# Optimization experiments

Hardware: AMD Instinct MI355X
Metric: run time of the kernel (lower is better)

Reference implementation:

```python
import jax, jax.numpy as jnp
import numpy as np

NUM_HEADS = 16

def setup_inputs() -> dict:
    key = jax.random.key(0)
    ks = jax.random.split(key, 5)
    B, T, C = 2, 2048, 1024
    s = 0.02
    return {
        "x": jax.random.normal(ks[0], (B, T, C), dtype=jnp.float32),
        "attn_w": jax.random.normal(ks[1], (3 * C, C), dtype=jnp.float32) * s,
        "attn_b": jax.random.normal(ks[2], (3 * C,), dtype=jnp.float32) * s,
        "proj_w": jax.random.normal(ks[3], (C, C), dtype=jnp.float32) * s,
        "proj_b": jax.random.normal(ks[4], (C,), dtype=jnp.float32) * s,
    }

def reference(x, attn_w, attn_b, proj_w, proj_b):
    B, T, C = x.shape
    H = NUM_HEADS
    D = C // H
    # fused QKV projection (torch Linear: x @ W^T + b)
    qkv = x @ attn_w.T + attn_b                      # [B, T, 3C]
    q, k, v = jnp.split(qkv, 3, axis=-1)             # each [B, T, C]
    # split heads -> [B, H, T, D]
    def heads(t):
        return t.reshape(B, T, H, D).transpose(0, 2, 1, 3)
    q, k, v = heads(q), heads(k), heads(v)
    scale = 1.0 / jnp.sqrt(jnp.asarray(D, dtype=x.dtype))
    scores = jnp.einsum("bhtd,bhsd->bhts", q, k) * scale   # [B, H, T, T]
    causal = jnp.tril(jnp.ones((T, T), dtype=bool))
    scores = jnp.where(causal[None, None], scores, jnp.asarray(-jnp.inf, dtype=scores.dtype))
    att = jax.nn.softmax(scores, axis=-1)
    out = jnp.einsum("bhts,bhsd->bhtd", att, v)      # [B, H, T, D]
    out = out.transpose(0, 2, 1, 3).reshape(B, T, C)
    return out @ proj_w.T + proj_b
```

## Files before the change

### kernel.cpp

```cpp
#include <hip/hip_runtime.h>
#include <hip/hip_bf16.h>

typedef __bf16 bf16_t;
typedef __bf16 bf16x4 __attribute__((ext_vector_type(4)));
typedef __bf16 bf16x8 __attribute__((ext_vector_type(8)));
typedef float f32x4 __attribute__((ext_vector_type(4)));
typedef float f32x8 __attribute__((ext_vector_type(8)));

#define MFMA16(a, b, c) __builtin_amdgcn_mfma_f32_16x16x32_bf16(a, b, c, 0, 0, 0)

#define GLOAD_LDS16(g, l)                                              \
  __builtin_amdgcn_global_load_lds(                                    \
      (const __attribute__((address_space(1))) unsigned int*)(g),      \
      (__attribute__((address_space(3))) unsigned int*)(l), 16, 0, 0)

constexpr int B = 2, T = 2048, C = 1024, H = 16, D = 64;
constexpr int NQKV = 3 * C;
constexpr int M = B * T;

#define QSCALE 0.18033688011112042f

struct LoOn  { static constexpr bool value = true;  };
struct LoOff { static constexpr bool value = false; };

__global__ __launch_bounds__(256) void cvt_kernel(
    const float* __restrict__ s0, bf16_t* __restrict__ d0, int n0,
    const float* __restrict__ s1, bf16_t* __restrict__ d1, int n1,
    const float* __restrict__ s2, bf16_t* __restrict__ d2, int n2)
{
  const float* s; bf16_t* d; int n;
  if (blockIdx.y == 0)      { s = s0; d = d0; n = n0; }
  else if (blockIdx.y == 1) { s = s1; d = d1; n = n1; }
  else                      { s = s2; d = d2; n = n2; }
  const int idx = (blockIdx.x * 256 + threadIdx.x) * 8;
  if (idx >= n) return;
  f32x8 t = *(const f32x8*)(s + idx);
  bf16x8 r;
#pragma unroll
  for (int j = 0; j < 8; ++j) r[j] = (bf16_t)t[j];
  *(bf16x8*)(d + idx) = r;
}

template<int BM, int BN, int MI, int NI, int WM, int WN>
__device__ __forceinline__ void gemm_mainloop_db(
    const bf16_t* __restrict__ A, const bf16_t* __restrict__ Wt,
    const int K, const int m0, const int n0,
    bf16_t* ldsA0, bf16_t* ldsA1, bf16_t* ldsB0, bf16_t* ldsB1,
    f32x4 acc[MI][NI])
{
  const int tid  = threadIdx.x;
  const int wv   = tid >> 6;
  const int lane = tid & 63;
  const int col  = lane & 15;
  const int quad = lane >> 4;
  const int lr8  = lane >> 3;
  const int cpos = lane & 7;
  const int wm = wv / WN, wn = wv % WN;
  constexpr int NW  = WM * WN;
  constexpr int ARW = BM / NW;
  constexpr int AJ  = ARW / 8;
  constexpr int BRW = BN / NW;
  constexpr int BJ  = BRW / 8;

  const bf16_t* ag[AJ]; const bf16_t* bg[BJ];
#pragma unroll
  for (int j = 0; j < AJ; ++j)
    ag[j] = A + (size_t)(m0 + wv * ARW + j * 8 + lr8) * K + (cpos ^ lr8) * 8;
#pragma unroll
  for (int j = 0; j < BJ; ++j)
    bg[j] = Wt + (size_t)(n0 + wv * BRW + j * 8 + lr8) * K + (cpos ^ lr8) * 8;

  const int xa = quad ^ (col & 7);
  const int niter = K / 64;

#pragma unroll
  for (int j = 0; j < AJ; ++j)
    GLOAD_LDS16(ag[j], ldsA0 + (wv * ARW + j * 8) * 64);
#pragma unroll
  for (int j = 0; j < BJ; ++j)
    GLOAD_LDS16(bg[j], ldsB0 + (wv * BRW + j * 8) * 64);

  for (int it = 0; it < niter; ++it) {
    __syncthreads();
    const bf16_t* cA = (it & 1) ? ldsA1 : ldsA0;
    const bf16_t* cB = (it & 1) ? ldsB1 : ldsB0;
    if (it + 1 < niter) {
      bf16_t* nA = (it & 1) ? ldsA0 : ldsA1;
      bf16_t* nB = (it & 1) ? ldsB0 : ldsB1;
      const int off = (it + 1) * 64;
#pragma unroll
      for (int j = 0; j < AJ; ++j)
        GLOAD_LDS16(ag[j] + off, nA + (wv * ARW + j * 8) * 64);
#pragma unroll
      for (int j = 0; j < BJ; ++j)
        GLOAD_LDS16(bg[j] + off, nB + (wv * BRW + j * 8) * 64);
    }
#pragma unroll
    for (int ks = 0; ks < 2; ++ks) {
      const int xk = (xa ^ (ks * 4)) * 8;
      bf16x8 af[MI], bfr[NI];
#pragma unroll
      for (int mi = 0; mi < MI; ++mi)
        af[mi] = *(const bf16x8*)(cA + (wm * (MI * 16) + mi * 16 + col) * 64 + xk);
#pragma unroll
      for (int ni = 0; ni < NI; ++ni)
        bfr[ni] = *(const bf16x8*)(cB + (wn * (NI * 16) + ni * 16 + col) * 64 + xk);
#pragma unroll
      for (int mi = 0; mi < MI; ++mi)
#pragma unroll
        for (int ni = 0; ni < NI; ++ni)
          acc[mi][ni] = MFMA16(af[mi], bfr[ni], acc[mi][ni]);
    }
  }
}

__global__ __launch_bounds__(256) void qkv_gemm_kernel(
    const bf16_t* __restrict__ x, const bf16_t* __restrict__ w,
    const float* __restrict__ bias,
    bf16_t* __restrict__ qws, bf16_t* __restrict__ kws, bf16_t* __restrict__ vws)
{
  __shared__ __align__(16) bf16_t ldsA[2][128 * 64];
  __shared__ __align__(16) bf16_t ldsB[2][128 * 64];
  const unsigned id = blockIdx.x;
  const unsigned lo = id & 7;
  const unsigned hi = id >> 3;
  const unsigned bx = hi % 24;
  const unsigned by = lo + 8 * (hi / 24);
  const int lane = threadIdx.x & 63;
  const int wv   = threadIdx.x >> 6;
  const int col  = lane & 15;
  const int quad = lane >> 4;
  const int wm = wv >> 1, wn = wv & 1;
  const int m0 = by * 128;
  const int n0 = bx * 128;

  f32x4 acc[4][4] = {};
  gemm_mainloop_db<128, 128, 4, 4, 2, 2>(x, w, C, m0, n0,
                                         ldsA[0], ldsA[1], ldsB[0], ldsB[1], acc);

  const int which = n0 >> 10;

  if (which == 2) {
    __syncthreads();
    bf16_t* vt = &ldsA[0][0] + wv * 4096;

#pragma unroll
    for (int ni = 0; ni < 4; ++ni) {
      const int n = n0 + wn * 64 + ni * 16 + col;
      const float bval = bias[n];
      const int dl = ni * 16 + col;
#pragma unroll
      for (int r = 0; r < 4; ++r) {
        bf16x4 pw;
#pragma unroll
        for (int mi = 0; mi < 4; ++mi)
          pw[mi] = (bf16_t)(acc[mi][ni][r] + bval);
        const int k = 2 * quad + (r >> 1);
        const int S = dl * 8 + (k ^ (dl & 7));
        *(bf16x4*)(vt + S * 8 + (r & 1) * 4) = pw;
      }
    }

    const int b   = (m0 + wm * 64) >> 11;
    const int t0w = (m0 + wm * 64) & (T - 1);
    const int h   = ((n0 + wn * 64) & (C - 1)) >> 6;
    const size_t bh = (size_t)(b * H + h);
    const int lr8 = lane >> 3;
    const int c8  = lane & 7;
#pragma unroll
    for (int j = 0; j < 8; ++j) {
      const int dl = j * 8 + lr8;
      const int d  = dl;
      bf16x8 row = *(const bf16x8*)(vt + (dl * 8 + (c8 ^ (dl & 7))) * 8);
      *(bf16x8*)(vws + (bh * D + d) * T + t0w + c8 * 8) = row;
    }
  } else {
#pragma unroll
    for (int ni = 0; ni < 4; ++ni) {
      const int n = n0 + wn * 64 + ni * 16 + col;
      const float bval = bias[n];
      const int c = n & (C - 1);
      const int h = c >> 6;
      const int d = c & 63;
#pragma unroll
      for (int mi = 0; mi < 4; ++mi) {
#pragma unroll
        for (int r = 0; r < 4; ++r) {
          const int m = m0 + wm * 64 + mi * 16 + quad * 4 + r;
          const int b = m >> 11;
          const int t = m & (T - 1);
          const size_t bh = (size_t)(b * H + h);
          if (which == 0)
            qws[(bh * T + t) * D + d] = (bf16_t)((acc[mi][ni][r] + bval) * QSCALE);
          else
            kws[(bh * T + t) * D + d] = (bf16_t)(acc[mi][ni][r] + bval);
        }
      }
    }
  }
}

__global__ __launch_bounds__(256) void attn_kernel(
    const bf16_t* __restrict__ qws, const bf16_t* __restrict__ kws,
    const bf16_t* __restrict__ vws, bf16_t* __restrict__ yws)
{
  const unsigned id = blockIdx.x;
  const int bh = (id & 7) + 8 * (id >> 7);
  const int pr = (id >> 3) & 15;
  const int tid  = threadIdx.x;
  const int wv   = tid >> 6;
  const int lane = tid & 63;
  const int col  = lane & 15;
  const int quad = lane >> 4;

  const bf16_t* Q  = qws + (size_t)bh * T * D;
  const bf16_t* K  = kws + (size_t)bh * T * D;
  const bf16_t* Vt = vws + (size_t)bh * D * T;

  __shared__ __align__(16) bf16_t ldsK[2][64 * 64];
  __shared__ __align__(16) bf16_t ldsV[2][64 * 64];
  __shared__ __align__(16) bf16_t ldsPh_s[4][16 * 64];
  __shared__ __align__(16) bf16_t ldsPl_s[4][16 * 64];
  bf16_t* ldsPh = ldsPh_s[wv];
  bf16_t* ldsPl = ldsPl_s[wv];

  const int xs   = col & 7;
  const int cxq  = (quad ^ xs) * 8;
  const int lr8  = lane >> 3;
  const int ksrc = (lane & 7) ^ lr8;
  const int pxor = (quad & 1) * 4;
  const int b = bh >> 4;
  const int h = bh & 15;

  const int qt_h = 31 - pr, qt_l = pr;
  const int t0h = qt_h * 64, t0l = qt_l * 64;
  const int twh = t0h + 16 * wv, twl = t0l + 16 * wv;

  bf16x8 qfh0 = *(const bf16x8*)(Q + (size_t)(twh + col) * D + quad * 8);
  bf16x8 qfh1 = *(const bf16x8*)(Q + (size_t)(twh + col) * D + 32 + quad * 8);
  bf16x8 qfl0 = *(const bf16x8*)(Q + (size_t)(twl + col) * D + quad * 8);
  bf16x8 qfl1 = *(const bf16x8*)(Q + (size_t)(twl + col) * D + 32 + quad * 8);

  f32x4 oh[4] = {}, ol[4] = {};
  f32x4 lph = {}, lpl = {};

  auto stage = [&](int it) {
    const int sn = it * 64;
    bf16_t* dK = ldsK[it & 1];
    bf16_t* dV = ldsV[it & 1];
#pragma unroll
    for (int j = 0; j < 2; ++j) {
      GLOAD_LDS16(K + (size_t)(sn + 16 * wv + j * 8 + lr8) * D + ksrc * 8,
                  dK + (16 * wv + j * 8) * 64);
      GLOAD_LDS16(Vt + (size_t)(16 * wv + j * 8 + lr8) * T + sn + ksrc * 8,
                  dV + (16 * wv + j * 8) * 64);
    }
  };

  auto body = [&](auto LOC, const bf16_t* bK, const bf16_t* bV,
                  int s0, bool hdiag, bool ldiag) {
    constexpr bool LO = decltype(LOC)::value;
    f32x4 sch[4], scl[4];
    __builtin_amdgcn_s_setprio(1);
#pragma unroll
    for (int kb = 0; kb < 4; ++kb) {
      const bf16_t* kr = bK + (kb * 16 + col) * 64;
      bf16x8 kf0 = *(const bf16x8*)(kr + cxq);
      bf16x8 kf1 = *(const bf16x8*)(kr + (cxq ^ 32));
      f32x4 a = {};
      a = MFMA16(qfh0, kf0, a);
      a = MFMA16(qfh1, kf1, a);
      sch[kb] = a;
      if constexpr (LO) {
        f32x4 c = {};
        c = MFMA16(qfl0, kf0, c);
        c = MFMA16(qfl1, kf1, c);
        scl[kb] = c;
      }
    }
    __builtin_amdgcn_s_setprio(0);
#pragma unroll
    for (int r = 0; r < 4; ++r) {
      const int prow = (quad * 4 + r) * 64;
      const int pxr  = pxor + r;
      const int poff = prow + (((col >> 1) ^ pxr) * 8) + (col & 1) * 4;
      bf16x4 pw;
#pragma unroll
      for (int kb = 0; kb < 4; ++kb) {
        float p = __builtin_amdgcn_exp2f(sch[kb][r]);
        if (hdiag && (s0 + kb * 16 + col > twh + quad * 4 + r)) p = 0.0f;
        lph[r] += p;
        pw[kb] = (bf16_t)p;
      }
      *(bf16x4*)(ldsPh + poff) = pw;
      if constexpr (LO) {
        bf16x4 pl;
#pragma unroll
        for (int kb = 0; kb < 4; ++kb) {
          float p = __builtin_amdgcn_exp2f(scl[kb][r]);
          if (ldiag && (s0 + kb * 16 + col > twl + quad * 4 + r)) p = 0.0f;
          lpl[r] += p;
          pl[kb] = (bf16_t)p;
        }
        *(bf16x4*)(ldsPl + poff) = pl;
      }
    }
    __builtin_amdgcn_s_setprio(1);
#pragma unroll
    for (int ks = 0; ks < 2; ++ks) {
      const int xk = cxq ^ (ks * 32);
      bf16x8 pah = *(const bf16x8*)(ldsPh + col * 64 + xk);
      bf16x8 pal{};
      if constexpr (LO) pal = *(const bf16x8*)(ldsPl + col * 64 + xk);
#pragma unroll
      for (int ni = 0; ni < 4; ++ni) {
        bf16x8 vf = *(const bf16x8*)(bV + (ni * 16 + col) * 64 + xk);
        oh[ni] = MFMA16(pah, vf, oh[ni]);
        if constexpr (LO) ol[ni] = MFMA16(pal, vf, ol[ni]);
      }
    }
    __builtin_amdgcn_s_setprio(0);
  };

  stage(0);

  for (int it = 0; it < qt_l; ++it) {
    __syncthreads();
    stage(it + 1);
    body(LoOn{}, ldsK[it & 1], ldsV[it & 1], it * 64, false, false);
  }
  {
    const int it = qt_l;
    __syncthreads();
    stage(it + 1);
    body(LoOn{}, ldsK[it & 1], ldsV[it & 1], it * 64, false, true);
  }
  for (int it = qt_l + 1; it < qt_h; ++it) {
    __syncthreads();
    stage(it + 1);
    body(LoOff{}, ldsK[it & 1], ldsV[it & 1], it * 64, false, false);
  }
  {
    __syncthreads();
    body(LoOff{}, ldsK[qt_h & 1], ldsV[qt_h & 1], qt_h * 64, true, false);
  }

#pragma unroll
  for (int r = 0; r < 4; ++r) {
    float l0 = lph[r], l1 = lpl[r];
#pragma unroll
    for (int off = 1; off < 16; off <<= 1) {
      l0 += __shfl_xor(l0, off);
      l1 += __shfl_xor(l1, off);
    }
    const float rl0 = 1.0f / l0, rl1 = 1.0f / l1;
    const int th = twh + quad * 4 + r;
    const int tl = twl + quad * 4 + r;
#pragma unroll
    for (int ni = 0; ni < 4; ++ni) {
      const int d = ni * 16 + col;
      yws[((size_t)(b * T + th)) * C + h * D + d] = (bf16_t)(oh[ni][r] * rl0);
      yws[((size_t)(b * T + tl)) * C + h * D + d] = (bf16_t)(ol[ni][r] * rl1);
    }
  }
}

__global__ __launch_bounds__(256) void proj_gemm_kernel(
    const bf16_t* __restrict__ y, const bf16_t* __restrict__ w,
    const float* __restrict__ bias, float* __restrict__ out)
{
  __shared__ __align__(16) bf16_t ldsA[2][128 * 64];
  __shared__ __align__(16) bf16_t ldsB[2][64 * 64];
  const unsigned id = blockIdx.x;
  const unsigned lo = id & 7;
  const unsigned hi = id >> 3;
  const unsigned bx = hi & 15;
  const unsigned by = lo + 8 * (hi >> 4);
  const int lane = threadIdx.x & 63;
  const int wv   = threadIdx.x >> 6;
  const int col  = lane & 15;
  const int quad = lane >> 4;
  const int wm = wv >> 1, wn = wv & 1;
  const int m0 = by * 128;
  const int n0 = bx * 64;

  f32x4 acc[4][2] = {};
  gemm_mainloop_db<128, 64, 4, 2, 2, 2>(y, w, C, m0, n0,
                                        ldsA[0], ldsA[1], ldsB[0], ldsB[1], acc);

#pragma unroll
  for (int ni = 0; ni < 2; ++ni) {
    const int n = n0 + wn * 32 + ni * 16 + col;
    const float bval = bias[n];
#pragma unroll
    for (int mi = 0; mi < 4; ++mi) {
#pragma unroll
      for (int r = 0; r < 4; ++r) {
        const int m = m0 + wm * 64 + mi * 16 + quad * 4 + r;
        out[(size_t)m * C + n] = acc[mi][ni][r] + bval;
      }
    }
  }
}

extern "C" void kernel_launch(void* const* d_in, const int* in_sizes, int n_in,
                              void* d_out, int out_size, void* d_ws, size_t ws_size,
                              hipStream_t stream) {
  const float* x      = (const float*)d_in[0];
  const float* attn_w = (const float*)d_in[1];
  const float* attn_b = (const float*)d_in[2];
  const float* proj_w = (const float*)d_in[3];
  const float* proj_b = (const float*)d_in[4];
  float* out = (float*)d_out;

  const size_t E = (size_t)B * H * T * D;
  char* ws = (char*)d_ws;
  bf16_t* qws = (bf16_t*)(ws);
  bf16_t* kws = (bf16_t*)(ws + 2 * E);
  bf16_t* vws = (bf16_t*)(ws + 4 * E);
  bf16_t* yws = (bf16_t*)(ws + 6 * E);
  bf16_t* xb  = (bf16_t*)(ws + 8 * E);
  bf16_t* awb = (bf16_t*)(ws + 10 * E);
  bf16_t* pwb = (bf16_t*)(ws + 11 * E + E / 2);

  const int NX = M * C, NAW = NQKV * C, NPW = C * C;
  cvt_kernel<<<dim3(NX / 2048, 3), 256, 0, stream>>>(
      x, xb, NX, attn_w, awb, NAW, proj_w, pwb, NPW);
  qkv_gemm_kernel<<<768, 256, 0, stream>>>(xb, awb, attn_b, qws, kws, vws);
  attn_kernel<<<512, 256, 0, stream>>>(qws, kws, vws, yws);
  proj_gemm_kernel<<<512, 256, 0, stream>>>(yws, pwb, proj_b, out);
}
```

Measured before the change: 163.8 us.

## Split attention KV range across two blocks per tile pair with combine kernel

The attention grid doubles from 512 to 1024 blocks. Each paired high/low query tile's KV range is split in two, so the first block handles the low tile plus the first half of the high tile's keys and the second block handles the rest. Partial unnormalized outputs and row sums for the high tile go to fp32 workspace buffers, and a new combine kernel merges them and writes bf16 output. The aim is more parallelism and better load balance across CUs, and the P staging buffer in LDS is halved. In exchange it adds an extra kernel launch and fp32 partial-result traffic.

```diff
diff --git a/kernel.cpp b/kernel.cpp
--- a/kernel.cpp
+++ b/kernel.cpp
@@ -20,8 +20,8 @@
 
 #define QSCALE 0.18033688011112042f
 
-struct LoOn  { static constexpr bool value = true;  };
-struct LoOff { static constexpr bool value = false; };
+struct TOn  { static constexpr bool value = true;  };
+struct TOff { static constexpr bool value = false; };
 
 __global__ __launch_bounds__(256) void cvt_kernel(
     const float* __restrict__ s0, bf16_t* __restrict__ d0, int n0,
@@ -202,11 +202,13 @@
 
 __global__ __launch_bounds__(256) void attn_kernel(
     const bf16_t* __restrict__ qws, const bf16_t* __restrict__ kws,
-    const bf16_t* __restrict__ vws, bf16_t* __restrict__ yws)
+    const bf16_t* __restrict__ vws, bf16_t* __restrict__ yws,
+    float* __restrict__ obuf, float* __restrict__ lbuf)
 {
   const unsigned id = blockIdx.x;
-  const int bh = (id & 7) + 8 * (id >> 7);
+  const int bh = (id & 7) + 8 * (id >> 8);
   const int pr = (id >> 3) & 15;
+  const int s  = (id >> 7) & 1;
   const int tid  = threadIdx.x;
   const int wv   = tid >> 6;
   const int lane = tid & 63;
@@ -219,10 +221,8 @@
 
   __shared__ __align__(16) bf16_t ldsK[2][64 * 64];
   __shared__ __align__(16) bf16_t ldsV[2][64 * 64];
-  __shared__ __align__(16) bf16_t ldsPh_s[4][16 * 64];
-  __shared__ __align__(16) bf16_t ldsPl_s[4][16 * 64];
-  bf16_t* ldsPh = ldsPh_s[wv];
-  bf16_t* ldsPl = ldsPl_s[wv];
+  __shared__ __align__(16) bf16_t ldsP_s[4][16 * 64];
+  bf16_t* ldsPw = ldsP_s[wv];
 
   const int xs   = col & 7;
   const int cxq  = (quad ^ xs) * 8;
@@ -233,8 +233,8 @@
   const int h = bh & 15;
 
   const int qt_h = 31 - pr, qt_l = pr;
-  const int t0h = qt_h * 64, t0l = qt_l * 64;
-  const int twh = t0h + 16 * wv, twl = t0l + 16 * wv;
+  const int h0   = 15 - pr;
+  const int twh = qt_h * 64 + 16 * wv, twl = qt_l * 64 + 16 * wv;
 
   bf16x8 qfh0 = *(const bf16x8*)(Q + (size_t)(twh + col) * D + quad * 8);
   bf16x8 qfh1 = *(const bf16x8*)(Q + (size_t)(twh + col) * D + 32 + quad * 8);
@@ -257,8 +257,9 @@
     }
   };
 
-  auto body = [&](auto LOC, const bf16_t* bK, const bf16_t* bV,
+  auto body = [&](auto HIC, auto LOC, const bf16_t* bK, const bf16_t* bV,
                   int s0, bool hdiag, bool ldiag) {
+    constexpr bool HI = decltype(HIC)::value;
     constexpr bool LO = decltype(LOC)::value;
     f32x4 sch[4], scl[4];
     __builtin_amdgcn_s_setprio(1);
@@ -267,10 +268,12 @@
       const bf16_t* kr = bK + (kb * 16 + col) * 64;
       bf16x8 kf0 = *(const bf16x8*)(kr + cxq);
       bf16x8 kf1 = *(const bf16x8*)(kr + (cxq ^ 32));
-      f32x4 a = {};
-      a = MFMA16(qfh0, kf0, a);
-      a = MFMA16(qfh1, kf1, a);
-      sch[kb] = a;
+      if constexpr (HI) {
+        f32x4 a = {};
+        a = MFMA16(qfh0, kf0, a);
+        a = MFMA16(qfh1, kf1, a);
+        sch[kb] = a;
+      }
       if constexpr (LO) {
         f32x4 c = {};
         c = MFMA16(qfl0, kf0, c);
@@ -279,90 +282,156 @@
       }
     }
     __builtin_amdgcn_s_setprio(0);
-#pragma unroll
-    for (int r = 0; r < 4; ++r) {
-      const int prow = (quad * 4 + r) * 64;
-      const int pxr  = pxor + r;
-      const int poff = prow + (((col >> 1) ^ pxr) * 8) + (col & 1) * 4;
-      bf16x4 pw;
-#pragma unroll
-      for (int kb = 0; kb < 4; ++kb) {
-        float p = __builtin_amdgcn_exp2f(sch[kb][r]);
-        if (hdiag && (s0 + kb * 16 + col > twh + quad * 4 + r)) p = 0.0f;
-        lph[r] += p;
-        pw[kb] = (bf16_t)p;
-      }
-      *(bf16x4*)(ldsPh + poff) = pw;
-      if constexpr (LO) {
-        bf16x4 pl;
+    if constexpr (HI) {
+#pragma unroll
+      for (int r = 0; r < 4; ++r) {
+        const int poff = (quad * 4 + r) * 64 +
+                         (((col >> 1) ^ (pxor + r)) * 8) + (col & 1) * 4;
+        bf16x4 pw;
+#pragma unroll
+        for (int kb = 0; kb < 4; ++kb) {
+          float p = __builtin_amdgcn_exp2f(sch[kb][r]);
+          if (hdiag && (s0 + kb * 16 + col > twh + quad * 4 + r)) p = 0.0f;
+          lph[r] += p;
+          pw[kb] = (bf16_t)p;
+        }
+        *(bf16x4*)(ldsPw + poff) = pw;
+      }
+      __builtin_amdgcn_s_setprio(1);
+#pragma unroll
+      for (int ks = 0; ks < 2; ++ks) {
+        const int xk = cxq ^ (ks * 32);
+        bf16x8 pa = *(const bf16x8*)(ldsPw + col * 64 + xk);
+#pragma unroll
+        for (int ni = 0; ni < 4; ++ni) {
+          bf16x8 vf = *(const bf16x8*)(bV + (ni * 16 + col) * 64 + xk);
+          oh[ni] = MFMA16(pa, vf, oh[ni]);
+        }
+      }
+      __builtin_amdgcn_s_setprio(0);
+    }
+    if constexpr (LO) {
+#pragma unroll
+      for (int r = 0; r < 4; ++r) {
+        const int poff = (quad * 4 + r) * 64 +
+                         (((col >> 1) ^ (pxor + r)) * 8) + (col & 1) * 4;
+        bf16x4 pw;
 #pragma unroll
         for (int kb = 0; kb < 4; ++kb) {
           float p = __builtin_amdgcn_exp2f(scl[kb][r]);
           if (ldiag && (s0 + kb * 16 + col > twl + quad * 4 + r)) p = 0.0f;
           lpl[r] += p;
-          pl[kb] = (bf16_t)p;
+          pw[kb] = (bf16_t)p;
         }
-        *(bf16x4*)(ldsPl + poff) = pl;
-      }
-    }
-    __builtin_amdgcn_s_setprio(1);
-#pragma unroll
-    for (int ks = 0; ks < 2; ++ks) {
-      const int xk = cxq ^ (ks * 32);
-      bf16x8 pah = *(const bf16x8*)(ldsPh + col * 64 + xk);
-      bf16x8 pal{};
-      if constexpr (LO) pal = *(const bf16x8*)(ldsPl + col * 64 + xk);
+        *(bf16x4*)(ldsPw + poff) = pw;
+      }
+      __builtin_amdgcn_s_setprio(1);
+#pragma unroll
+      for (int ks = 0; ks < 2; ++ks) {
+        const int xk = cxq ^ (ks * 32);
+        bf16x8 pa = *(const bf16x8*)(ldsPw + col * 64 + xk);
+#pragma unroll
+        for (int ni = 0; ni < 4; ++ni) {
+          bf16x8 vf = *(const bf16x8*)(bV + (ni * 16 + col) * 64 + xk);
+          ol[ni] = MFMA16(pa, vf, ol[ni]);
+        }
+      }
+      __builtin_amdgcn_s_setprio(0);
+    }
+  };
+
+  if (s == 0) {
+    const int stmax = (qt_l > h0 - 1) ? qt_l : (h0 - 1);
+    stage(0);
+    int it = 0;
+    const int nBoth = (h0 < qt_l + 1) ? h0 : (qt_l + 1);
+    const bool bothDiag = (qt_l < h0);
+    for (; it < nBoth - (bothDiag ? 1 : 0); ++it) {
+      __syncthreads();
+      if (it + 1 <= stmax) stage(it + 1);
+      body(TOn{}, TOn{}, ldsK[it & 1], ldsV[it & 1], it * 64, false, false);
+    }
+    if (bothDiag) {
+      __syncthreads();
+      if (it + 1 <= stmax) stage(it + 1);
+      body(TOn{}, TOn{}, ldsK[it & 1], ldsV[it & 1], it * 64, false, true);
+      ++it;
+      for (; it < h0; ++it) {
+        __syncthreads();
+        if (it + 1 <= stmax) stage(it + 1);
+        body(TOn{}, TOff{}, ldsK[it & 1], ldsV[it & 1], it * 64, false, false);
+      }
+    } else {
+      for (; it < qt_l; ++it) {
+        __syncthreads();
+        if (it + 1 <= stmax) stage(it + 1);
+        body(TOff{}, TOn{}, ldsK[it & 1], ldsV[it & 1], it * 64, false, false);
+      }
+      __syncthreads();
+      body(TOff{}, TOn{}, ldsK[it & 1], ldsV[it & 1], it * 64, false, true);
+    }
+  } else {
+    stage(h0);
+    int it = h0;
+    for (; it < qt_h; ++it) {
+      __syncthreads();
+      stage(it + 1);
+      body(TOn{}, TOff{}, ldsK[it & 1], ldsV[it & 1], it * 64, false, false);
+    }
+    __syncthreads();
+    body(TOn{}, TOff{}, ldsK[it & 1], ldsV[it & 1], it * 64, true, false);
+  }
+
+  {
+    float* ob = obuf + (size_t)s * (B * H * 1024 * D);
+    float* lb = lbuf + s * (B * H * 1024);
+    const int orow = bh * 1024;
+#pragma unroll
+    for (int r = 0; r < 4; ++r) {
+      float lh = lph[r];
+#pragma unroll
+      for (int off = 1; off < 16; off <<= 1) lh += __shfl_xor(lh, off);
+      const int tt = twh + quad * 4 + r - 1024;
+      if ((lane & 15) == 0) lb[orow + tt] = lh;
+#pragma unroll
+      for (int ni = 0; ni < 4; ++ni)
+        ob[(size_t)(orow + tt) * D + ni * 16 + col] = oh[ni][r];
+    }
+  }
+  if (s == 0) {
+#pragma unroll
+    for (int r = 0; r < 4; ++r) {
+      float l1 = lpl[r];
+#pragma unroll
+      for (int off = 1; off < 16; off <<= 1) l1 += __shfl_xor(l1, off);
+      const float rl1 = 1.0f / l1;
+      const int tl = twl + quad * 4 + r;
 #pragma unroll
       for (int ni = 0; ni < 4; ++ni) {
-        bf16x8 vf = *(const bf16x8*)(bV + (ni * 16 + col) * 64 + xk);
-        oh[ni] = MFMA16(pah, vf, oh[ni]);
-        if constexpr (LO) ol[ni] = MFMA16(pal, vf, ol[ni]);
-      }
-    }
-    __builtin_amdgcn_s_setprio(0);
-  };
-
-  stage(0);
-
-  for (int it = 0; it < qt_l; ++it) {
-    __syncthreads();
-    stage(it + 1);
-    body(LoOn{}, ldsK[it & 1], ldsV[it & 1], it * 64, false, false);
+        const int d = ni * 16 + col;
+        yws[((size_t)(b * T + tl)) * C + h * D + d] = (bf16_t)(ol[ni][r] * rl1);
+      }
+    }
   }
-  {
-    const int it = qt_l;
-    __syncthreads();
-    stage(it + 1);
-    body(LoOn{}, ldsK[it & 1], ldsV[it & 1], it * 64, false, true);
-  }
-  for (int it = qt_l + 1; it < qt_h; ++it) {
-    __syncthreads();
-    stage(it + 1);
-    body(LoOff{}, ldsK[it & 1], ldsV[it & 1], it * 64, false, false);
-  }
-  {
-    __syncthreads();
-    body(LoOff{}, ldsK[qt_h & 1], ldsV[qt_h & 1], qt_h * 64, true, false);
-  }
-
-#pragma unroll
-  for (int r = 0; r < 4; ++r) {
-    float l0 = lph[r], l1 = lpl[r];
-#pragma unroll
-    for (int off = 1; off < 16; off <<= 1) {
-      l0 += __shfl_xor(l0, off);
-      l1 += __shfl_xor(l1, off);
-    }
-    const float rl0 = 1.0f / l0, rl1 = 1.0f / l1;
-    const int th = twh + quad * 4 + r;
-    const int tl = twl + quad * 4 + r;
-#pragma unroll
-    for (int ni = 0; ni < 4; ++ni) {
-      const int d = ni * 16 + col;
-      yws[((size_t)(b * T + th)) * C + h * D + d] = (bf16_t)(oh[ni][r] * rl0);
-      yws[((size_t)(b * T + tl)) * C + h * D + d] = (bf16_t)(ol[ni][r] * rl1);
-    }
-  }
+}
+
+__global__ __launch_bounds__(256) void attn_combine_kernel(
+    const float* __restrict__ obuf, const float* __restrict__ lbuf,
+    bf16_t* __restrict__ yws)
+{
+  constexpr int NO = B * H * 1024 * D;
+  constexpr int NL = B * H * 1024;
+  const int i8 = (blockIdx.x * 256 + threadIdx.x) * 8;
+  const int row = i8 >> 6;
+  const int bh = row >> 10, tt = row & 1023;
+  const float rl = 1.0f / (lbuf[row] + lbuf[NL + row]);
+  f32x8 a = *(const f32x8*)(obuf + i8);
+  f32x8 c = *(const f32x8*)(obuf + NO + i8);
+  bf16x8 yv;
+#pragma unroll
+  for (int j = 0; j < 8; ++j) yv[j] = (bf16_t)((a[j] + c[j]) * rl);
+  const int b = bh >> 4, h = bh & 15;
+  *(bf16x8*)(yws + ((size_t)(b * T + 1024 + tt)) * C + h * D + (i8 & 63)) = yv;
 }
 
 __global__ __launch_bounds__(256) void proj_gemm_kernel(
@@ -422,11 +491,15 @@
   bf16_t* xb  = (bf16_t*)(ws + 8 * E);
   bf16_t* awb = (bf16_t*)(ws + 10 * E);
   bf16_t* pwb = (bf16_t*)(ws + 11 * E + E / 2);
+  float*  obuf = (float*)(ws + 12 * E);
+  float*  lbuf = (float*)(ws + 16 * E);
 
   const int NX = M * C, NAW = NQKV * C, NPW = C * C;
   cvt_kernel<<<dim3(NX / 2048, 3), 256, 0, stream>>>(
       x, xb, NX, attn_w, awb, NAW, proj_w, pwb, NPW);
   qkv_gemm_kernel<<<768, 256, 0, stream>>>(xb, awb, attn_b, qws, kws, vws);
-  attn_kernel<<<512, 256, 0, stream>>>(qws, kws, vws, yws);
+  attn_kernel<<<1024, 256, 0, stream>>>(qws, kws, vws, yws, obuf, lbuf);
+  attn_combine_kernel<<<(B * H * 1024 * D) / 2048, 256, 0, stream>>>(
+      obuf, lbuf, yws);
   proj_gemm_kernel<<<512, 256, 0, stream>>>(yws, pwb, proj_b, out);
 }
```

After: 169.7 us. +3.6%, slower.
